# Optimization experiments

Measured on AMD Instinct MI355X. Metric: run time of the kernel, lower is better.

The kernel has to match this reference:

```python
import jax, jax.numpy as jnp
from jax import lax
import numpy as np

BETA = 6.6


def _conv(x, w, b=None, stride=1, pad=0):
    # x: NCHW, w: OIHW (torch layout)
    y = lax.conv_general_dilated(x, w, (stride, stride), [(pad, pad), (pad, pad)],
                                 dimension_numbers=('NCHW', 'OIHW', 'NCHW'))
    if b is not None:
        y = y + b[None, :, None, None]
    return y


def _conv_t(x, w, b, stride=2, pad=1):
    # torch ConvTranspose2d: w is [in, out, kH, kW]; equivalent to dilated conv with flipped kernel
    k = w.shape[2]
    w2 = jnp.flip(w, (2, 3)).transpose(1, 0, 2, 3)  # -> OIHW
    y = lax.conv_general_dilated(x, w2, (1, 1), [(k - 1 - pad, k - 1 - pad)] * 2,
                                 lhs_dilation=(stride, stride),
                                 dimension_numbers=('NCHW', 'OIHW', 'NCHW'))
    return y + b[None, :, None, None]


def _res_stack(x, pairs):
    for wa, wb in pairs:
        x = x + _conv(jax.nn.relu(_conv(jax.nn.relu(x), wa, pad=1)), wb, pad=1)
    return jax.nn.relu(x)


def _quantize(z, E, beta):
    # z: [B, D, H, W]; E: [K, D]
    xp = z.transpose(0, 2, 3, 1)                       # BHWD
    flat = xp.reshape(-1, E.shape[1])                  # [N, D]
    d = (jnp.sum(flat ** 2, axis=1, keepdims=True)
         + jnp.sum(E ** 2, axis=1)
         - 2.0 * flat @ E.T)                           # [N, K]
    idx = jnp.argmin(d, axis=1)                        # [N]
    q = E[idx].reshape(xp.shape)                       # gather == onehot @ E
    loss_q = jnp.mean((q - lax.stop_gradient(xp)) ** 2)
    loss_e = jnp.mean((lax.stop_gradient(q) - xp) ** 2)
    loss = loss_q + beta * loss_e
    q_st = xp + lax.stop_gradient(q - xp)              # straight-through
    z_q = q_st.transpose(0, 3, 1, 2)
    counts = jnp.zeros((E.shape[0],), jnp.float32).at[idx].add(1.0)
    probs = counts / flat.shape[0]
    perplexity = jnp.exp(-jnp.sum(probs * jnp.log(probs + 1e-10)))
    return loss, z_q, perplexity


def setup_inputs() -> dict:
    key = jax.random.key(0)
    ks = iter(jax.random.split(key, 32))

    def p(*s):
        return jax.random.normal(next(ks), s, jnp.float32) * 0.05

    inp = dict(
        x=jax.random.normal(next(ks), (32, 3, 256, 256), jnp.float32),
        # encoder
        w1=p(64, 3, 4, 4), b1=p(64),
        w2=p(128, 64, 4, 4), b2=p(128),
        w3=p(128, 128, 3, 3), b3=p(128),
        r0a=p(32, 128, 3, 3), r0b=p(128, 32, 3, 3),
        r1a=p(32, 128, 3, 3), r1b=p(128, 32, 3, 3),
        # pre-VQ 1x1 conv
        wp=p(64, 128, 1, 1), bp=p(64),
        # codebook
        E=jax.random.uniform(next(ks), (512, 64), jnp.float32, -1.0 / 512, 1.0 / 512),
        # decoder
        dw1=p(128, 64, 3, 3), db1=p(128),
        dr0a=p(32, 128, 3, 3), dr0b=p(128, 32, 3, 3),
        dr1a=p(32, 128, 3, 3), dr1b=p(128, 32, 3, 3),
        tw1=p(128, 64, 4, 4), tb1=p(64),   # ConvTranspose2d(128,64,4,2,1) torch layout [in,out,k,k]
        tw2=p(64, 3, 4, 4), tb2=p(3),      # ConvTranspose2d(64,3,4,2,1)
    )
    return inp


def reference(x, w1, b1, w2, b2, w3, b3, r0a, r0b, r1a, r1b, wp, bp, E,
              dw1, db1, dr0a, dr0b, dr1a, dr1b, tw1, tb1, tw2, tb2):
    # Encoder
    z = jax.nn.relu(_conv(x, w1, b1, stride=2, pad=1))
    z = jax.nn.relu(_conv(z, w2, b2, stride=2, pad=1))
    z = _conv(z, w3, b3, stride=1, pad=1)
    z = _res_stack(z, [(r0a, r0b), (r1a, r1b)])
    # pre-VQ projection
    z = _conv(z, wp, bp)
    # Vector quantization
    loss, z_q, perplexity = _quantize(z, E, BETA)
    # Decoder
    d = _conv(z_q, dw1, db1, pad=1)
    d = _res_stack(d, [(dr0a, dr0b), (dr1a, dr1b)])
    d = jax.nn.relu(_conv_t(d, tw1, tb1))
    x_tilda = _conv_t(d, tw2, tb2)
    return (loss, x_tilda, perplexity)
```

## Files before the change

### kernel.cpp

```cpp
#include <hip/hip_runtime.h>
#include <math.h>

typedef __attribute__((ext_vector_type(8))) short bf16x8;
typedef __attribute__((ext_vector_type(4))) float f32x4;

__device__ inline float bf2f(ushort u) {
    union { uint i; float f; } v; v.i = ((uint)u) << 16; return v.f;
}
__device__ inline ushort f2bf(float f) {
    union { float f; uint i; } v; v.f = f;
    uint b = v.i;
    b += 0x7FFFu + ((b >> 16) & 1u);
    return (ushort)(b >> 16);
}
__device__ inline uint relu2bf(uint x) {
    uint s = x & 0x80008000u;
    uint m = (s >> 15) * 0xFFFFu;
    return x & ~m;
}

template<int CIN, int COUT, int NT>
__global__ __launch_bounds__(256) void wt_oihw(const float* __restrict__ s, ushort* __restrict__ d) {
    int i = blockIdx.x * 256 + threadIdx.x;
    if (i >= COUT * NT * CIN) return;
    int co = i / (NT * CIN);
    int r  = i % (NT * CIN);
    int tap = r / CIN, ci = r % CIN;
    d[i] = f2bf(s[(co * CIN + ci) * NT + tap]);
}

__global__ __launch_bounds__(256) void wt_tconv1(const float* __restrict__ s, ushort* __restrict__ d) {
    int i = blockIdx.x * 256 + threadIdx.x;
    if (i >= 4 * 64 * 512) return;
    int cls = i >> 15;
    int co  = (i >> 9) & 63;
    int k   = i & 511;
    int tap = k >> 7, ci = k & 127;
    int a = tap >> 1, b = tap & 1;
    int ph = cls >> 1, pw = cls & 1;
    int kh = ph ? (a ? 2 : 0) : (a ? 3 : 1);
    int kw = pw ? (b ? 2 : 0) : (b ? 3 : 1);
    d[i] = f2bf(s[((ci * 64 + co) << 4) + kh * 4 + kw]);
}

__global__ __launch_bounds__(256) void vq_prep(const float* __restrict__ E,
                                               ushort* __restrict__ Ebf, float* __restrict__ eN) {
    int i = blockIdx.x * 256 + threadIdx.x;
    if (i < 32768) Ebf[i] = f2bf(E[i]);
    if (i < 512) {
        float s = 0.f;
        #pragma unroll 8
        for (int d = 0; d < 64; ++d) { float x = E[i * 64 + d]; s = fmaf(x, x, s); }
        eN[i] = s;
    }
}

template<int CIN, int COUT, int S, int CFG, int CLS, int NT,
         bool RELU_A, bool RELU_OUT, bool HAS_RES>
__global__ __launch_bounds__(256)
void conv_mfma2(const ushort* __restrict__ in, const ushort* __restrict__ wt,
                const float* __restrict__ bias, const ushort* __restrict__ res,
                ushort* __restrict__ out, int Hin, int Win) {
    constexpr int K = NT * CIN;
    constexpr int KSTEPS = K / 32;
    constexpr int CSTEPS = CIN / 32;
    constexpr int WM = (COUT == 128) ? 4 : 2;
    constexpr int WN = (COUT == 32) ? 2 : 4;

    __shared__ ushort sA[2][128 * 40];

    const int t = threadIdx.x;
    const int w = t >> 6, l = t & 63;
    const int bid = blockIdx.x;
    const int n = bid >> 5, R = bid & 31;

    const int m0 = (COUT == 128) ? 64 * (w >> 1) : 32 * w;
    const int n0 = (COUT == 128) ? 64 * (w & 1) : 0;

    const int gpx  = t >> 1;
    const int gk   = (t & 1) * 16;
    const int grow = 2 * R + (gpx >> 6);
    const int gcol = gpx & 63;

    auto gather = [&](int ks, uint4& g0, uint4& g1) {
        int tap, ci0;
        if (CSTEPS == 1) { tap = ks; ci0 = 0; }
        else             { tap = ks / CSTEPS; ci0 = (ks % CSTEPS) * 32; }
        int dh, dw;
        if (CFG == 0)      { dh = tap / 3 - 1; dw = tap % 3 - 1; }
        else if (CFG == 1) { dh = tap / 4 - 1; dw = tap % 4 - 1; }
        else if (CFG == 2) { int a = tap >> 1, b = tap & 1;
                             dh = (CLS >> 1) ? 1 - a : -a;
                             dw = (CLS & 1) ? 1 - b : -b; }
        else               { dh = 0; dw = 0; }
        const int ih = S * grow + dh, iw = S * gcol + dw;
        g0 = make_uint4(0u, 0u, 0u, 0u); g1 = g0;
        if ((unsigned)ih < (unsigned)Hin && (unsigned)iw < (unsigned)Win) {
            const ushort* p = in + (((long long)(n * Hin + ih)) * Win + iw) * CIN + ci0 + gk;
            g0 = *reinterpret_cast<const uint4*>(p);
            g1 = *reinterpret_cast<const uint4*>(p + 8);
        }
        if (RELU_A) {
            g0.x = relu2bf(g0.x); g0.y = relu2bf(g0.y); g0.z = relu2bf(g0.z); g0.w = relu2bf(g0.w);
            g1.x = relu2bf(g1.x); g1.y = relu2bf(g1.y); g1.z = relu2bf(g1.z); g1.w = relu2bf(g1.w);
        }
    };

    f32x4 acc[WM][WN] = {};

    uint4 g0, g1;
    gather(0, g0, g1);
    *reinterpret_cast<uint4*>(&sA[0][gpx * 40 + gk])     = g0;
    *reinterpret_cast<uint4*>(&sA[0][gpx * 40 + gk + 8]) = g1;
    __syncthreads();

    int cur = 0;
    for (int ks = 0; ks < KSTEPS; ++ks) {
        const bool more = (ks + 1 < KSTEPS);
        uint4 h0, h1;
        if (more) gather(ks + 1, h0, h1);

        bf16x8 bfr[WN];
        #pragma unroll
        for (int nf = 0; nf < WN; ++nf)
            bfr[nf] = *reinterpret_cast<const bf16x8*>(
                wt + (n0 + nf * 16 + (l & 15)) * K + ks * 32 + ((l >> 4) * 8));

        bf16x8 afr[WM];
        #pragma unroll
        for (int mf = 0; mf < WM; ++mf)
            afr[mf] = *reinterpret_cast<const bf16x8*>(
                &sA[cur][(m0 + mf * 16 + (l & 15)) * 40 + ((l >> 4) * 8)]);

        #pragma unroll
        for (int mf = 0; mf < WM; ++mf)
            #pragma unroll
            for (int nf = 0; nf < WN; ++nf)
                acc[mf][nf] = __builtin_amdgcn_mfma_f32_16x16x32_bf16(
                    afr[mf], bfr[nf], acc[mf][nf], 0, 0, 0);

        if (more) {
            *reinterpret_cast<uint4*>(&sA[cur ^ 1][gpx * 40 + gk])     = h0;
            *reinterpret_cast<uint4*>(&sA[cur ^ 1][gpx * 40 + gk + 8]) = h1;
            __syncthreads();
            cur ^= 1;
        }
    }

    #pragma unroll
    for (int mf = 0; mf < WM; ++mf) {
        #pragma unroll
        for (int nf = 0; nf < WN; ++nf) {
            const int col = n0 + nf * 16 + (l & 15);
            const float bv = bias ? bias[col] : 0.f;
            #pragma unroll
            for (int r = 0; r < 4; ++r) {
                const int prow = m0 + mf * 16 + ((l >> 4) * 4) + r;
                const int orow = 2 * R + (prow >> 6);
                const int ocol = prow & 63;
                long long oidx;
                if (CFG == 2)
                    oidx = (((long long)(n * 128 + 2 * orow + (CLS >> 1))) * 128
                            + 2 * ocol + (CLS & 1)) * COUT + col;
                else
                    oidx = (((long long)(n * 64 + orow)) * 64 + ocol) * COUT + col;
                float v = acc[mf][nf][r] + bv;
                if (HAS_RES) v += bf2f(res[oidx]);
                if (RELU_OUT) v = fmaxf(v, 0.f);
                out[oidx] = f2bf(v);
            }
        }
    }
}

__global__ __launch_bounds__(256)
void conv1_k(const float* __restrict__ x, const float* __restrict__ w1,
             const float* __restrict__ b1, ushort* __restrict__ out) {
    __shared__ float sIn[3 * 4 * 36];
    __shared__ float sW[64 * 48];
    const int t = threadIdx.x;
    const int bid = blockIdx.x;
    const int n = bid >> 7, oh = bid & 127;
    const int ow0 = blockIdx.y * 16;

    for (int i = t; i < 3072; i += 256) sW[i] = w1[i];
    for (int i = t; i < 3 * 4 * 34; i += 256) {
        int ci = i / 136, r = i - ci * 136;
        int r4 = r / 34, iwl = r % 34;
        int ih = 2 * oh - 1 + r4;
        int iw = 2 * ow0 - 1 + iwl;
        float v = 0.f;
        if ((unsigned)ih < 256u && (unsigned)iw < 256u)
            v = x[((n * 3 + ci) * 256 + ih) * 256 + iw];
        sIn[ci * 144 + r4 * 36 + iwl] = v;
    }
    __syncthreads();

    const int co = t & 63, j = t >> 6;
    float wr[48];
    #pragma unroll
    for (int i = 0; i < 48; ++i) wr[i] = sW[co * 48 + i];
    const float bv = b1[co];

    #pragma unroll
    for (int q = 0; q < 4; ++q) {
        const int owl = j * 4 + q;
        float acc = bv;
        #pragma unroll
        for (int ci = 0; ci < 3; ++ci)
            #pragma unroll
            for (int kh = 0; kh < 4; ++kh)
                #pragma unroll
                for (int kw = 0; kw < 4; ++kw)
                    acc = fmaf(sIn[ci * 144 + kh * 36 + 2 * owl + kw],
                               wr[ci * 16 + kh * 4 + kw], acc);
        acc = fmaxf(acc, 0.f);
        out[(((long long)(n * 128 + oh)) * 128 + ow0 + owl) * 64 + co] = f2bf(acc);
    }
}

__global__ __launch_bounds__(256)
void convt2_k(const ushort* __restrict__ in, const float* __restrict__ tw2,
              const float* __restrict__ tb2, float* __restrict__ out) {
    __shared__ float sW[64 * 48];
    const int t = threadIdx.x;
    for (int i = t; i < 3072; i += 256) sW[i] = tw2[i];
    __syncthreads();

    const int bid = blockIdx.x;
    const int n = bid >> 8, oh = bid & 255;
    const int ow = t;
    const int khA = (oh + 1) & 1, ihA = (oh + 1) >> 1;
    const int kwA = (ow + 1) & 1, iwA = (ow + 1) >> 1;

    float a0 = tb2[0], a1 = tb2[1], a2 = tb2[2];
    #pragma unroll
    for (int a = 0; a < 2; ++a) {
        const int ih = ihA - a;
        if ((unsigned)ih >= 128u) continue;
        const int kh = khA + 2 * a;
        #pragma unroll
        for (int b = 0; b < 2; ++b) {
            const int iw = iwA - b;
            if ((unsigned)iw >= 128u) continue;
            const int kw = kwA + 2 * b;
            const ushort* src = in + (((long long)(n * 128 + ih)) * 128 + iw) * 64;
            const int k = kh * 4 + kw;
            #pragma unroll
            for (int c8 = 0; c8 < 8; ++c8) {
                uint4 v = *reinterpret_cast<const uint4*>(src + c8 * 8);
                const uint u[4] = {v.x, v.y, v.z, v.w};
                #pragma unroll
                for (int p = 0; p < 4; ++p) {
                    union { uint i; float f; } lo, hi;
                    lo.i = u[p] << 16; hi.i = u[p] & 0xFFFF0000u;
                    const int ci = c8 * 8 + p * 2;
                    a0 = fmaf(lo.f, sW[ci * 48 + 0 * 16 + k], a0);
                    a1 = fmaf(lo.f, sW[ci * 48 + 1 * 16 + k], a1);
                    a2 = fmaf(lo.f, sW[ci * 48 + 2 * 16 + k], a2);
                    a0 = fmaf(hi.f, sW[(ci + 1) * 48 + 0 * 16 + k], a0);
                    a1 = fmaf(hi.f, sW[(ci + 1) * 48 + 1 * 16 + k], a1);
                    a2 = fmaf(hi.f, sW[(ci + 1) * 48 + 2 * 16 + k], a2);
                }
            }
        }
    }
    const long long px = (long long)oh * 256 + ow;
    out[(long long)(n * 3 + 0) * 65536 + px] = a0;
    out[(long long)(n * 3 + 1) * 65536 + px] = a1;
    out[(long long)(n * 3 + 2) * 65536 + px] = a2;
}

__global__ __launch_bounds__(256)
void vq_mfma(const ushort* __restrict__ z, const ushort* __restrict__ Ebf,
             const float* __restrict__ E, const float* __restrict__ eN,
             ushort* __restrict__ zq, float* __restrict__ stats) {
    __shared__ ushort sZ[64 * 72];
    __shared__ float sEN[512];
    __shared__ float sV[64 * 4];
    __shared__ int   sI[64 * 4];
    __shared__ int   sIdx[64];
    __shared__ unsigned shist[512];
    __shared__ float red[256];

    const int t = threadIdx.x;
    const int w = t >> 6, l = t & 63;
    const long long p0 = (long long)blockIdx.x * 64;

    {
        const int px = t >> 2, koff = (t & 3) * 16;
        const ushort* p = z + (p0 + px) * 64 + koff;
        uint4 a0 = *reinterpret_cast<const uint4*>(p);
        uint4 a1 = *reinterpret_cast<const uint4*>(p + 8);
        *reinterpret_cast<uint4*>(&sZ[px * 72 + koff])     = a0;
        *reinterpret_cast<uint4*>(&sZ[px * 72 + koff + 8]) = a1;
        sEN[t] = eN[t]; sEN[t + 256] = eN[t + 256];
        shist[t] = 0u; shist[t + 256] = 0u;
    }
    __syncthreads();

    f32x4 acc[4][8] = {};
    #pragma unroll
    for (int ks = 0; ks < 2; ++ks) {
        bf16x8 bfr[8];
        #pragma unroll
        for (int nf = 0; nf < 8; ++nf)
            bfr[nf] = *reinterpret_cast<const bf16x8*>(
                Ebf + (w * 128 + nf * 16 + (l & 15)) * 64 + ks * 32 + ((l >> 4) * 8));
        #pragma unroll
        for (int mf = 0; mf < 4; ++mf) {
            bf16x8 afr = *reinterpret_cast<const bf16x8*>(
                &sZ[(mf * 16 + (l & 15)) * 72 + ks * 32 + ((l >> 4) * 8)]);
            #pragma unroll
            for (int nf = 0; nf < 8; ++nf)
                acc[mf][nf] = __builtin_amdgcn_mfma_f32_16x16x32_bf16(
                    afr, bfr[nf], acc[mf][nf], 0, 0, 0);
        }
    }

    float eNr[8];
    #pragma unroll
    for (int nf = 0; nf < 8; ++nf) eNr[nf] = sEN[w * 128 + nf * 16 + (l & 15)];

    #pragma unroll
    for (int mf = 0; mf < 4; ++mf) {
        #pragma unroll
        for (int r = 0; r < 4; ++r) {
            float best = 3.4e38f; int bidx = 0;
            #pragma unroll
            for (int nf = 0; nf < 8; ++nf) {
                float s = eNr[nf] - 2.f * acc[mf][nf][r];
                int   c = w * 128 + nf * 16 + (l & 15);
                if (s < best || (s == best && c < bidx)) { best = s; bidx = c; }
            }
            #pragma unroll
            for (int off = 1; off < 16; off <<= 1) {
                float ov = __shfl_xor(best, off);
                int   oi = __shfl_xor(bidx, off);
                if (ov < best || (ov == best && oi < bidx)) { best = ov; bidx = oi; }
            }
            if ((l & 15) == 0) {
                const int px = mf * 16 + ((l >> 4) * 4) + r;
                sV[px * 4 + w] = best; sI[px * 4 + w] = bidx;
            }
        }
    }
    __syncthreads();

    if (t < 64) {
        float best = sV[t * 4]; int bidx = sI[t * 4];
        #pragma unroll
        for (int w2 = 1; w2 < 4; ++w2) {
            float v = sV[t * 4 + w2]; int c = sI[t * 4 + w2];
            if (v < best || (v == best && c < bidx)) { best = v; bidx = c; }
        }
        sIdx[t] = bidx;
        atomicAdd(&shist[bidx], 1u);
    }
    __syncthreads();

    {
        const int px = t >> 2, doff = (t & 3) * 16;
        const int idx = sIdx[px];
        const float* e = E + idx * 64 + doff;
        float dist = 0.f;
        uint4 pk4[2];
        ushort* pk = reinterpret_cast<ushort*>(pk4);
        #pragma unroll
        for (int j = 0; j < 16; ++j) {
            float ev = e[j];
            float zv = bf2f(sZ[px * 72 + doff + j]);
            float df = ev - zv;
            dist = fmaf(df, df, dist);
            pk[j] = f2bf(ev);
        }
        *reinterpret_cast<uint4*>(zq + (p0 + px) * 64 + doff)     = pk4[0];
        *reinterpret_cast<uint4*>(zq + (p0 + px) * 64 + doff + 8) = pk4[1];
        red[t] = dist;
    }
    __syncthreads();
    for (int s = 128; s > 0; s >>= 1) {
        if (t < s) red[t] += red[t + s];
        __syncthreads();
    }
    if (t == 0) atomicAdd(&stats[0], red[0]);
    for (int i = t; i < 512; i += 256) {
        unsigned c = shist[i];
        if (c) atomicAdd(&stats[1 + i], (float)c);
    }
}

__global__ __launch_bounds__(512)
void finalize_kernel(const float* __restrict__ stats, float* __restrict__ out, int plast) {
    __shared__ float red[512];
    int t = threadIdx.x;
    float c = stats[1 + t];
    float p = c * (1.f / 131072.f);
    red[t] = p * logf(p + 1e-10f);
    __syncthreads();
    for (int s = 256; s > 0; s >>= 1) {
        if (t < s) red[t] += red[t + s];
        __syncthreads();
    }
    if (t == 0) {
        out[plast] = expf(-red[0]);
        out[0] = 7.6f * stats[0] * (1.f / 8388608.f);
    }
}

extern "C" void kernel_launch(void* const* d_in, const int* in_sizes, int n_in,
                              void* d_out, int out_size, void* d_ws, size_t ws_size,
                              hipStream_t stream) {
    (void)in_sizes; (void)n_in; (void)ws_size;
    const float* x   = (const float*)d_in[0];
    const float* w1  = (const float*)d_in[1];
    const float* b1  = (const float*)d_in[2];
    const float* w2  = (const float*)d_in[3];
    const float* b2  = (const float*)d_in[4];
    const float* w3  = (const float*)d_in[5];
    const float* b3  = (const float*)d_in[6];
    const float* r0a = (const float*)d_in[7];
    const float* r0b = (const float*)d_in[8];
    const float* r1a = (const float*)d_in[9];
    const float* r1b = (const float*)d_in[10];
    const float* wp  = (const float*)d_in[11];
    const float* bp  = (const float*)d_in[12];
    const float* E   = (const float*)d_in[13];
    const float* dw1 = (const float*)d_in[14];
    const float* db1 = (const float*)d_in[15];
    const float* dr0a= (const float*)d_in[16];
    const float* dr0b= (const float*)d_in[17];
    const float* dr1a= (const float*)d_in[18];
    const float* dr1b= (const float*)d_in[19];
    const float* tw1 = (const float*)d_in[20];
    const float* tb1 = (const float*)d_in[21];
    const float* tw2 = (const float*)d_in[22];
    const float* tb2 = (const float*)d_in[23];

    float* out = (float*)d_out;
    ushort* ws = (ushort*)d_ws;

    ushort* H1 = ws;
    ushort* H2 = ws + 33554432;
    ushort* C  = ws + 50331648;
    ushort* F  = ws + 67108864;
    ushort* Z  = ws + 71303168;
    ushort* ZQ = ws + 79691776;
    ushort* W0 = ws + 88080384;
    ushort* Wt2   = W0;
    ushort* Wt3   = W0 + 131072;
    ushort* Wr0a  = W0 + 278528;
    ushort* Wr0b  = W0 + 315392;
    ushort* Wr1a  = W0 + 352256;
    ushort* Wr1b  = W0 + 389120;
    ushort* Wp    = W0 + 425984;
    ushort* Wd1   = W0 + 434176;
    ushort* Wdr0a = W0 + 507904;
    ushort* Wdr0b = W0 + 544768;
    ushort* Wdr1a = W0 + 581632;
    ushort* Wdr1b = W0 + 618496;
    ushort* WT1   = W0 + 655360;
    ushort* Ebf   = W0 + 786432;
    float*  eN    = (float*)(W0 + 819200);
    float*  ST    = (float*)(W0 + 820224);
    ushort* T = H1;
    ushort* D = H2;

    hipMemsetAsync(ST, 0, 513 * sizeof(float), stream);

    dim3 blk(256);
    wt_oihw<64, 128,16><<<512, blk, 0, stream>>>(w2,  Wt2);
    wt_oihw<128,128, 9><<<576, blk, 0, stream>>>(w3,  Wt3);
    wt_oihw<128, 32, 9><<<144, blk, 0, stream>>>(r0a, Wr0a);
    wt_oihw<32, 128, 9><<<144, blk, 0, stream>>>(r0b, Wr0b);
    wt_oihw<128, 32, 9><<<144, blk, 0, stream>>>(r1a, Wr1a);
    wt_oihw<32, 128, 9><<<144, blk, 0, stream>>>(r1b, Wr1b);
    wt_oihw<128, 64, 1><<<32,  blk, 0, stream>>>(wp,  Wp);
    wt_oihw<64, 128, 9><<<288, blk, 0, stream>>>(dw1, Wd1);
    wt_oihw<128, 32, 9><<<144, blk, 0, stream>>>(dr0a, Wdr0a);
    wt_oihw<32, 128, 9><<<144, blk, 0, stream>>>(dr0b, Wdr0b);
    wt_oihw<128, 32, 9><<<144, blk, 0, stream>>>(dr1a, Wdr1a);
    wt_oihw<32, 128, 9><<<144, blk, 0, stream>>>(dr1b, Wdr1b);
    wt_tconv1<<<512, blk, 0, stream>>>(tw1, WT1);
    vq_prep<<<128, blk, 0, stream>>>(E, Ebf, eN);

    conv1_k<<<dim3(32 * 128, 8), blk, 0, stream>>>(x, w1, b1, H1);
    conv_mfma2<64,128,2,1,0,16,false,true ,false><<<1024, blk, 0, stream>>>(H1, Wt2, b2, nullptr, H2, 128, 128);
    conv_mfma2<128,128,1,0,0, 9,false,false,false><<<1024, blk, 0, stream>>>(H2, Wt3, b3, nullptr, C, 64, 64);
    conv_mfma2<128, 32,1,0,0, 9,true ,true ,false><<<1024, blk, 0, stream>>>(C, Wr0a, nullptr, nullptr, F, 64, 64);
    conv_mfma2<32, 128,1,0,0, 9,false,false,true ><<<1024, blk, 0, stream>>>(F, Wr0b, nullptr, C, C, 64, 64);
    conv_mfma2<128, 32,1,0,0, 9,true ,true ,false><<<1024, blk, 0, stream>>>(C, Wr1a, nullptr, nullptr, F, 64, 64);
    conv_mfma2<32, 128,1,0,0, 9,false,true ,true ><<<1024, blk, 0, stream>>>(F, Wr1b, nullptr, C, C, 64, 64);
    conv_mfma2<128, 64,1,3,0, 1,false,false,false><<<1024, blk, 0, stream>>>(C, Wp, bp, nullptr, Z, 64, 64);

    vq_mfma<<<2048, blk, 0, stream>>>(Z, Ebf, E, eN, ZQ, ST);

    conv_mfma2<64,128,1,0,0, 9,false,false,false><<<1024, blk, 0, stream>>>(ZQ, Wd1, db1, nullptr, D, 64, 64);
    conv_mfma2<128, 32,1,0,0, 9,true ,true ,false><<<1024, blk, 0, stream>>>(D, Wdr0a, nullptr, nullptr, F, 64, 64);
    conv_mfma2<32, 128,1,0,0, 9,false,false,true ><<<1024, blk, 0, stream>>>(F, Wdr0b, nullptr, D, D, 64, 64);
    conv_mfma2<128, 32,1,0,0, 9,true ,true ,false><<<1024, blk, 0, stream>>>(D, Wdr1a, nullptr, nullptr, F, 64, 64);
    conv_mfma2<32, 128,1,0,0, 9,false,true ,true ><<<1024, blk, 0, stream>>>(F, Wdr1b, nullptr, D, D, 64, 64);
    conv_mfma2<128, 64,1,2,0, 4,false,true ,false><<<1024, blk, 0, stream>>>(D, WT1 + 0 * 32768, tb1, nullptr, T, 64, 64);
    conv_mfma2<128, 64,1,2,1, 4,false,true ,false><<<1024, blk, 0, stream>>>(D, WT1 + 1 * 32768, tb1, nullptr, T, 64, 64);
    conv_mfma2<128, 64,1,2,2, 4,false,true ,false><<<1024, blk, 0, stream>>>(D, WT1 + 2 * 32768, tb1, nullptr, T, 64, 64);
    conv_mfma2<128, 64,1,2,3, 4,false,true ,false><<<1024, blk, 0, stream>>>(D, WT1 + 3 * 32768, tb1, nullptr, T, 64, 64);
    convt2_k<<<32 * 256, blk, 0, stream>>>(T, tw2, tb2, out + 1);

    finalize_kernel<<<1, 512, 0, stream>>>(ST, out, out_size - 1);
}
```

Baseline: 1.328 ms.

## Stage input tile with halo in LDS once per block for implicit-GEMM convs

Stride-1 convolutions now load the block's input rows plus a one-pixel halo into shared memory once, then read A fragments for every tap from LDS. This replaces the per-k-step global gather with double buffering and removes about nine-fold redundant global reads. The four transposed-conv phase launches are merged into one kernel where each wave handles one output phase and all share the LDS tile. conv1's weight staging is also transposed for conflict-free LDS reads. The cost is larger LDS use per block, which may lower occupancy, and no overlap between the global load and the MFMA work.

Result: faster. 1.256 ms (-5.4%).

```diff
diff --git a/kernel.cpp b/kernel.cpp
--- a/kernel.cpp
+++ b/kernel.cpp
@@ -55,19 +55,23 @@
     }
 }
 
-template<int CIN, int COUT, int S, int CFG, int CLS, int NT,
-         bool RELU_A, bool RELU_OUT, bool HAS_RES>
+template<int CIN, int COUT, int NT, int HALO, bool RELU_A, bool RELU_OUT, bool HAS_RES>
 __global__ __launch_bounds__(256)
-void conv_mfma2(const ushort* __restrict__ in, const ushort* __restrict__ wt,
-                const float* __restrict__ bias, const ushort* __restrict__ res,
-                ushort* __restrict__ out, int Hin, int Win) {
+void conv_lds(const ushort* __restrict__ in, const ushort* __restrict__ wt,
+              const float* __restrict__ bias, const ushort* __restrict__ res,
+              ushort* __restrict__ out) {
     constexpr int K = NT * CIN;
     constexpr int KSTEPS = K / 32;
     constexpr int CSTEPS = CIN / 32;
+    constexpr int PR = HALO ? 4 : 2;
+    constexpr int PC = HALO ? 66 : 64;
+    constexpr int CIP = CIN + 8;
     constexpr int WM = (COUT == 128) ? 4 : 2;
     constexpr int WN = (COUT == 32) ? 2 : 4;
-
-    __shared__ ushort sA[2][128 * 40];
+    constexpr int NC8 = CIN / 8;
+    constexpr int NLD = PR * PC * NC8;
+
+    __shared__ ushort sP[PR * PC * CIP];
 
     const int t = threadIdx.x;
     const int w = t >> 6, l = t & 63;
@@ -77,6 +81,179 @@
     const int m0 = (COUT == 128) ? 64 * (w >> 1) : 32 * w;
     const int n0 = (COUT == 128) ? 64 * (w & 1) : 0;
 
+    for (int i = t; i < NLD; i += 256) {
+        const int c8  = i & (NC8 - 1);
+        const int rem = i / NC8;
+        const int pc  = rem % PC;
+        const int pr  = rem / PC;
+        const int grow = 2 * R - HALO + pr;
+        const int gcol = pc - HALO;
+        uint4 v = make_uint4(0u, 0u, 0u, 0u);
+        if (!HALO || ((unsigned)grow < 64u && (unsigned)gcol < 64u))
+            v = *reinterpret_cast<const uint4*>(
+                in + (((long long)(n * 64 + grow)) * 64 + gcol) * CIN + c8 * 8);
+        if (RELU_A) {
+            v.x = relu2bf(v.x); v.y = relu2bf(v.y);
+            v.z = relu2bf(v.z); v.w = relu2bf(v.w);
+        }
+        *reinterpret_cast<uint4*>(&sP[(pr * PC + pc) * CIP + c8 * 8]) = v;
+    }
+    __syncthreads();
+
+    int aoff[WM];
+    #pragma unroll
+    for (int mf = 0; mf < WM; ++mf) {
+        const int px = m0 + mf * 16 + (l & 15);
+        aoff[mf] = ((px >> 6) * PC + (px & 63)) * CIP + ((l >> 4) * 8);
+    }
+
+    f32x4 acc[WM][WN] = {};
+
+    for (int ks = 0; ks < KSTEPS; ++ks) {
+        const int tap = (CSTEPS == 1) ? ks : ks / CSTEPS;
+        const int ci0 = (CSTEPS == 1) ? 0 : (ks % CSTEPS) * 32;
+        int dh = 0, dw = 0;
+        if (NT == 9) { dh = tap / 3 - 1; dw = tap % 3 - 1; }
+        const int base = ((dh + HALO) * PC + (dw + HALO)) * CIP + ci0;
+
+        bf16x8 bfr[WN];
+        #pragma unroll
+        for (int nf = 0; nf < WN; ++nf)
+            bfr[nf] = *reinterpret_cast<const bf16x8*>(
+                wt + (n0 + nf * 16 + (l & 15)) * K + ks * 32 + ((l >> 4) * 8));
+
+        #pragma unroll
+        for (int mf = 0; mf < WM; ++mf) {
+            bf16x8 afr = *reinterpret_cast<const bf16x8*>(&sP[base + aoff[mf]]);
+            #pragma unroll
+            for (int nf = 0; nf < WN; ++nf)
+                acc[mf][nf] = __builtin_amdgcn_mfma_f32_16x16x32_bf16(
+                    afr, bfr[nf], acc[mf][nf], 0, 0, 0);
+        }
+    }
+
+    #pragma unroll
+    for (int mf = 0; mf < WM; ++mf) {
+        #pragma unroll
+        for (int nf = 0; nf < WN; ++nf) {
+            const int col = n0 + nf * 16 + (l & 15);
+            const float bv = bias ? bias[col] : 0.f;
+            #pragma unroll
+            for (int r = 0; r < 4; ++r) {
+                const int prow = m0 + mf * 16 + ((l >> 4) * 4) + r;
+                const int orow = 2 * R + (prow >> 6);
+                const int ocol = prow & 63;
+                const long long oidx = (((long long)(n * 64 + orow)) * 64 + ocol) * COUT + col;
+                float v = acc[mf][nf][r] + bv;
+                if (HAS_RES) v += bf2f(res[oidx]);
+                if (RELU_OUT) v = fmaxf(v, 0.f);
+                out[oidx] = f2bf(v);
+            }
+        }
+    }
+}
+
+__global__ __launch_bounds__(256)
+void convt1_lds(const ushort* __restrict__ in, const ushort* __restrict__ wt,
+                const float* __restrict__ bias, ushort* __restrict__ out) {
+    constexpr int CIN = 128, CIP = 136, PC = 66;
+    __shared__ ushort sP[4 * PC * CIP];
+
+    const int t = threadIdx.x;
+    const int w = t >> 6, l = t & 63;
+    const int bid = blockIdx.x;
+    const int n = bid >> 5, R = bid & 31;
+
+    for (int i = t; i < 4 * PC * 16; i += 256) {
+        const int c8  = i & 15;
+        const int rem = i >> 4;
+        const int pc  = rem % PC;
+        const int pr  = rem / PC;
+        const int grow = 2 * R - 1 + pr;
+        const int gcol = pc - 1;
+        uint4 v = make_uint4(0u, 0u, 0u, 0u);
+        if ((unsigned)grow < 64u && (unsigned)gcol < 64u)
+            v = *reinterpret_cast<const uint4*>(
+                in + (((long long)(n * 64 + grow)) * 64 + gcol) * CIN + c8 * 8);
+        *reinterpret_cast<uint4*>(&sP[(pr * PC + pc) * CIP + c8 * 8]) = v;
+    }
+    __syncthreads();
+
+    const int ph = w >> 1, pw = w & 1;
+    const ushort* wc = wt + w * 32768;
+
+    int aoff[8];
+    #pragma unroll
+    for (int mf = 0; mf < 8; ++mf) {
+        const int px = mf * 16 + (l & 15);
+        aoff[mf] = ((px >> 6) * PC + (px & 63)) * CIP + ((l >> 4) * 8);
+    }
+
+    f32x4 acc[8][4] = {};
+
+    for (int ks = 0; ks < 16; ++ks) {
+        const int tap = ks >> 2, ci0 = (ks & 3) * 32;
+        const int a = tap >> 1, b = tap & 1;
+        const int dh = ph ? 1 - a : -a;
+        const int dw = pw ? 1 - b : -b;
+        const int base = ((dh + 1) * PC + (dw + 1)) * CIP + ci0;
+
+        bf16x8 bfr[4];
+        #pragma unroll
+        for (int nf = 0; nf < 4; ++nf)
+            bfr[nf] = *reinterpret_cast<const bf16x8*>(
+                wc + (nf * 16 + (l & 15)) * 512 + ks * 32 + ((l >> 4) * 8));
+
+        #pragma unroll
+        for (int mf = 0; mf < 8; ++mf) {
+            bf16x8 afr = *reinterpret_cast<const bf16x8*>(&sP[base + aoff[mf]]);
+            #pragma unroll
+            for (int nf = 0; nf < 4; ++nf)
+                acc[mf][nf] = __builtin_amdgcn_mfma_f32_16x16x32_bf16(
+                    afr, bfr[nf], acc[mf][nf], 0, 0, 0);
+        }
+    }
+
+    #pragma unroll
+    for (int mf = 0; mf < 8; ++mf) {
+        #pragma unroll
+        for (int nf = 0; nf < 4; ++nf) {
+            const int col = nf * 16 + (l & 15);
+            const float bv = bias[col];
+            #pragma unroll
+            for (int r = 0; r < 4; ++r) {
+                const int prow = mf * 16 + ((l >> 4) * 4) + r;
+                const int orow = 2 * R + (prow >> 6);
+                const int ocol = prow & 63;
+                const long long oidx =
+                    (((long long)(n * 128 + 2 * orow + ph)) * 128 + 2 * ocol + pw) * 64 + col;
+                float v = fmaxf(acc[mf][nf][r] + bv, 0.f);
+                out[oidx] = f2bf(v);
+            }
+        }
+    }
+}
+
+template<int CIN, int COUT, bool RELU_OUT>
+__global__ __launch_bounds__(256)
+void conv_s2(const ushort* __restrict__ in, const ushort* __restrict__ wt,
+             const float* __restrict__ bias, ushort* __restrict__ out,
+             int Hin, int Win) {
+    constexpr int K = 16 * CIN;
+    constexpr int KSTEPS = K / 32;
+    constexpr int CSTEPS = CIN / 32;
+    constexpr int WM = 4, WN = 4;
+
+    __shared__ ushort sA[2][128 * 40];
+
+    const int t = threadIdx.x;
+    const int w = t >> 6, l = t & 63;
+    const int bid = blockIdx.x;
+    const int n = bid >> 5, R = bid & 31;
+
+    const int m0 = 64 * (w >> 1);
+    const int n0 = 64 * (w & 1);
+
     const int gpx  = t >> 1;
     const int gk   = (t & 1) * 16;
     const int grow = 2 * R + (gpx >> 6);
@@ -86,24 +263,14 @@
         int tap, ci0;
         if (CSTEPS == 1) { tap = ks; ci0 = 0; }
         else             { tap = ks / CSTEPS; ci0 = (ks % CSTEPS) * 32; }
-        int dh, dw;
-        if (CFG == 0)      { dh = tap / 3 - 1; dw = tap % 3 - 1; }
-        else if (CFG == 1) { dh = tap / 4 - 1; dw = tap % 4 - 1; }
-        else if (CFG == 2) { int a = tap >> 1, b = tap & 1;
-                             dh = (CLS >> 1) ? 1 - a : -a;
-                             dw = (CLS & 1) ? 1 - b : -b; }
-        else               { dh = 0; dw = 0; }
-        const int ih = S * grow + dh, iw = S * gcol + dw;
+        const int dh = tap / 4 - 1, dw = tap % 4 - 1;
+        const int ih = 2 * grow + dh, iw = 2 * gcol + dw;
         g0 = make_uint4(0u, 0u, 0u, 0u); g1 = g0;
         if ((unsigned)ih < (unsigned)Hin && (unsigned)iw < (unsigned)Win) {
             const ushort* p = in + (((long long)(n * Hin + ih)) * Win + iw) * CIN + ci0 + gk;
             g0 = *reinterpret_cast<const uint4*>(p);
             g1 = *reinterpret_cast<const uint4*>(p + 8);
         }
-        if (RELU_A) {
-            g0.x = relu2bf(g0.x); g0.y = relu2bf(g0.y); g0.z = relu2bf(g0.z); g0.w = relu2bf(g0.w);
-            g1.x = relu2bf(g1.x); g1.y = relu2bf(g1.y); g1.z = relu2bf(g1.z); g1.w = relu2bf(g1.w);
-        }
     };
 
     f32x4 acc[WM][WN] = {};
@@ -152,20 +319,14 @@
         #pragma unroll
         for (int nf = 0; nf < WN; ++nf) {
             const int col = n0 + nf * 16 + (l & 15);
-            const float bv = bias ? bias[col] : 0.f;
+            const float bv = bias[col];
             #pragma unroll
             for (int r = 0; r < 4; ++r) {
                 const int prow = m0 + mf * 16 + ((l >> 4) * 4) + r;
                 const int orow = 2 * R + (prow >> 6);
                 const int ocol = prow & 63;
-                long long oidx;
-                if (CFG == 2)
-                    oidx = (((long long)(n * 128 + 2 * orow + (CLS >> 1))) * 128
-                            + 2 * ocol + (CLS & 1)) * COUT + col;
-                else
-                    oidx = (((long long)(n * 64 + orow)) * 64 + ocol) * COUT + col;
+                const long long oidx = (((long long)(n * 64 + orow)) * 64 + ocol) * COUT + col;
                 float v = acc[mf][nf][r] + bv;
-                if (HAS_RES) v += bf2f(res[oidx]);
                 if (RELU_OUT) v = fmaxf(v, 0.f);
                 out[oidx] = f2bf(v);
             }
@@ -177,13 +338,16 @@
 void conv1_k(const float* __restrict__ x, const float* __restrict__ w1,
              const float* __restrict__ b1, ushort* __restrict__ out) {
     __shared__ float sIn[3 * 4 * 36];
-    __shared__ float sW[64 * 48];
+    __shared__ float sW[48 * 64];
     const int t = threadIdx.x;
     const int bid = blockIdx.x;
     const int n = bid >> 7, oh = bid & 127;
     const int ow0 = blockIdx.y * 16;
 
-    for (int i = t; i < 3072; i += 256) sW[i] = w1[i];
+    for (int i = t; i < 3072; i += 256) {
+        int co = i / 48, k = i % 48;
+        sW[k * 64 + co] = w1[i];
+    }
     for (int i = t; i < 3 * 4 * 34; i += 256) {
         int ci = i / 136, r = i - ci * 136;
         int r4 = r / 34, iwl = r % 34;
@@ -199,7 +363,7 @@
     const int co = t & 63, j = t >> 6;
     float wr[48];
     #pragma unroll
-    for (int i = 0; i < 48; ++i) wr[i] = sW[co * 48 + i];
+    for (int i = 0; i < 48; ++i) wr[i] = sW[i * 64 + co];
     const float bv = b1[co];
 
     #pragma unroll
@@ -485,25 +649,22 @@
     vq_prep<<<128, blk, 0, stream>>>(E, Ebf, eN);
 
     conv1_k<<<dim3(32 * 128, 8), blk, 0, stream>>>(x, w1, b1, H1);
-    conv_mfma2<64,128,2,1,0,16,false,true ,false><<<1024, blk, 0, stream>>>(H1, Wt2, b2, nullptr, H2, 128, 128);
-    conv_mfma2<128,128,1,0,0, 9,false,false,false><<<1024, blk, 0, stream>>>(H2, Wt3, b3, nullptr, C, 64, 64);
-    conv_mfma2<128, 32,1,0,0, 9,true ,true ,false><<<1024, blk, 0, stream>>>(C, Wr0a, nullptr, nullptr, F, 64, 64);
-    conv_mfma2<32, 128,1,0,0, 9,false,false,true ><<<1024, blk, 0, stream>>>(F, Wr0b, nullptr, C, C, 64, 64);
-    conv_mfma2<128, 32,1,0,0, 9,true ,true ,false><<<1024, blk, 0, stream>>>(C, Wr1a, nullptr, nullptr, F, 64, 64);
-    conv_mfma2<32, 128,1,0,0, 9,false,true ,true ><<<1024, blk, 0, stream>>>(F, Wr1b, nullptr, C, C, 64, 64);
-    conv_mfma2<128, 64,1,3,0, 1,false,false,false><<<1024, blk, 0, stream>>>(C, Wp, bp, nullptr, Z, 64, 64);
+    conv_s2<64,128,true><<<1024, blk, 0, stream>>>(H1, Wt2, b2, H2, 128, 128);
+    conv_lds<128,128,9,1,false,false,false><<<1024, blk, 0, stream>>>(H2, Wt3, b3, nullptr, C);
+    conv_lds<128, 32,9,1,true ,true ,false><<<1024, blk, 0, stream>>>(C, Wr0a, nullptr, nullptr, F);
+    conv_lds<32, 128,9,1,false,false,true ><<<1024, blk, 0, stream>>>(F, Wr0b, nullptr, C, C);
+    conv_lds<128, 32,9,1,true ,true ,false><<<1024, blk, 0, stream>>>(C, Wr1a, nullptr, nullptr, F);
+    conv_lds<32, 128,9,1,false,true ,true ><<<1024, blk, 0, stream>>>(F, Wr1b, nullptr, C, C);
+    conv_lds<128, 64,1,0,false,false,false><<<1024, blk, 0, stream>>>(C, Wp, bp, nullptr, Z);
 
     vq_mfma<<<2048, blk, 0, stream>>>(Z, Ebf, E, eN, ZQ, ST);
 
-    conv_mfma2<64,128,1,0,0, 9,false,false,false><<<1024, blk, 0, stream>>>(ZQ, Wd1, db1, nullptr, D, 64, 64);
-    conv_mfma2<128, 32,1,0,0, 9,true ,true ,false><<<1024, blk, 0, stream>>>(D, Wdr0a, nullptr, nullptr, F, 64, 64);
-    conv_mfma2<32, 128,1,0,0, 9,false,false,true ><<<1024, blk, 0, stream>>>(F, Wdr0b, nullptr, D, D, 64, 64);
-    conv_mfma2<128, 32,1,0,0, 9,true ,true ,false><<<1024, blk, 0, stream>>>(D, Wdr1a, nullptr, nullptr, F, 64, 64);
-    conv_mfma2<32, 128,1,0,0, 9,false,true ,true ><<<1024, blk, 0, stream>>>(F, Wdr1b, nullptr, D, D, 64, 64);
-    conv_mfma2<128, 64,1,2,0, 4,false,true ,false><<<1024, blk, 0, stream>>>(D, WT1 + 0 * 32768, tb1, nullptr, T, 64, 64);
-    conv_mfma2<128, 64,1,2,1, 4,false,true ,false><<<1024, blk, 0, stream>>>(D, WT1 + 1 * 32768, tb1, nullptr, T, 64, 64);
-    conv_mfma2<128, 64,1,2,2, 4,false,true ,false><<<1024, blk, 0, stream>>>(D, WT1 + 2 * 32768, tb1, nullptr, T, 64, 64);
-    conv_mfma2<128, 64,1,2,3, 4,false,true ,false><<<1024, blk, 0, stream>>>(D, WT1 + 3 * 32768, tb1, nullptr, T, 64, 64);
+    conv_lds<64, 128,9,1,false,false,false><<<1024, blk, 0, stream>>>(ZQ, Wd1, db1, nullptr, D);
+    conv_lds<128, 32,9,1,true ,true ,false><<<1024, blk, 0, stream>>>(D, Wdr0a, nullptr, nullptr, F);
+    conv_lds<32, 128,9,1,false,false,true ><<<1024, blk, 0, stream>>>(F, Wdr0b, nullptr, D, D);
+    conv_lds<128, 32,9,1,true ,true ,false><<<1024, blk, 0, stream>>>(D, Wdr1a, nullptr, nullptr, F);
+    conv_lds<32, 128,9,1,false,true ,true ><<<1024, blk, 0, stream>>>(F, Wdr1b, nullptr, D, D);
+    convt1_lds<<<1024, blk, 0, stream>>>(D, WT1, tb1, T);
     convt2_k<<<32 * 256, blk, 0, stream>>>(T, tw2, tb2, out + 1);
 
     finalize_kernel<<<1, 512, 0, stream>>>(ST, out, out_size - 1);
```
